# Optimization experiments

Measured on AMD Instinct MI355X. Metric: run time of the kernel, lower is better.

The kernel has to match this reference:

```python
import jax, jax.numpy as jnp
import numpy as np

B, T, D, H, C = 2048, 512, 1, 50, 2  # batch, seq_len, input_size, hidden_size, num_classes


def setup_inputs() -> dict:
    key = jax.random.key(0)
    ks = jax.random.split(key, 11)
    k = 1.0 / np.sqrt(H)  # torch default init bound
    u = lambda kk, shape: jax.random.uniform(kk, shape, jnp.float32, -k, k)
    return {
        "x": jax.random.normal(ks[0], (B, T, D), jnp.float32),
        "W_ih0": u(ks[1], (4 * H, D)),
        "W_hh0": u(ks[2], (4 * H, H)),
        "b_ih0": u(ks[3], (4 * H,)),
        "b_hh0": u(ks[4], (4 * H,)),
        "W_ih1": u(ks[5], (4 * H, H)),
        "W_hh1": u(ks[6], (4 * H, H)),
        "b_ih1": u(ks[7], (4 * H,)),
        "b_hh1": u(ks[8], (4 * H,)),
        "W_fc": u(ks[9], (C, H)),
        "b_fc": u(ks[10], (C,)),
    }


def _lstm_layer(x, Wih, Whh, bih, bhh):
    # x: [B, T, Din] -> hidden sequence [B, T, H]. PyTorch gate order: i, f, g, o.
    Bn = x.shape[0]
    Hn = Whh.shape[1]
    # precompute input contribution for all timesteps (one big GEMM)
    xg = jnp.einsum('btd,gd->btg', x, Wih) + bih + bhh  # [B, T, 4H]

    def step(carry, xg_t):
        h, c = carry
        g = xg_t + h @ Whh.T  # [B, 4H]
        i, f, gg, o = jnp.split(g, 4, axis=-1)
        i = jax.nn.sigmoid(i)
        f = jax.nn.sigmoid(f)
        gg = jnp.tanh(gg)
        o = jax.nn.sigmoid(o)
        c = f * c + i * gg
        h = o * jnp.tanh(c)
        return (h, c), h

    h0 = jnp.zeros((Bn, Hn), x.dtype)
    c0 = jnp.zeros((Bn, Hn), x.dtype)
    (_, _), hs = jax.lax.scan(step, (h0, c0), jnp.swapaxes(xg, 0, 1))  # hs: [T, B, H]
    return jnp.swapaxes(hs, 0, 1)


def reference(x, W_ih0, W_hh0, b_ih0, b_hh0, W_ih1, W_hh1, b_ih1, b_hh1, W_fc, b_fc):
    h1 = _lstm_layer(x, W_ih0, W_hh0, b_ih0, b_hh0)
    h2 = _lstm_layer(h1, W_ih1, W_hh1, b_ih1, b_hh1)
    # out[:, -1, :] @ W_fc.T + b_fc  (last-timestep hidden -> classifier)
    return h2[:, -1, :] @ W_fc.T + b_fc
```

## Files before the change

### kernel.cpp

```cpp
#include <hip/hip_runtime.h>

#define T_SEQ 512
#define HID   50
#define NB    8
#define BLK   832

typedef float v4f  __attribute__((ext_vector_type(4)));
typedef _Float16 f16;
typedef f16  f16x8 __attribute__((ext_vector_type(8)));


__device__ __forceinline__ f16x8 ldA0(const float* __restrict__ Whh0,
                                      const float* __restrict__ Wih0,
                                      const float* __restrict__ bih0,
                                      const float* __restrict__ bhh0,
                                      int m, int kb) {
    const int u = m >> 2, g = m & 3;
    f16x8 v;
    #pragma unroll
    for (int j = 0; j < 8; ++j) {
        const int k = kb + j;
        float f = 0.f;
        if (u < HID) {
            const int rho = g * HID + u;
            if (k < HID)      f = Whh0[rho * HID + k];
            else if (k == 62) f = Wih0[rho];
            else if (k == 63) f = bih0[rho] + bhh0[rho];
        }
        v[j] = (f16)f;
    }
    return v;
}

__device__ __forceinline__ f16x8 ldA1a(const float* __restrict__ Wih1,
                                       const float* __restrict__ bih1,
                                       const float* __restrict__ bhh1,
                                       int m, int kb) {
    const int u = m >> 2, g = m & 3;
    f16x8 v;
    #pragma unroll
    for (int j = 0; j < 8; ++j) {
        const int k = kb + j;
        float f = 0.f;
        if (u < HID) {
            const int rho = g * HID + u;
            if (k < HID)      f = Wih1[rho * HID + k];
            else if (k == 63) f = bih1[rho] + bhh1[rho];
        }
        v[j] = (f16)f;
    }
    return v;
}

__device__ __forceinline__ f16x8 ldA1b(const float* __restrict__ Whh1,
                                       int m, int kb) {
    const int u = m >> 2, g = m & 3;
    f16x8 v;
    #pragma unroll
    for (int j = 0; j < 8; ++j) {
        const int k = kb + j;
        float f = 0.f;
        if (u < HID && k < HID) f = Whh1[(g * HID + u) * HID + k];
        v[j] = (f16)f;
    }
    return v;
}

#define MFMA16(A, B, C) __builtin_amdgcn_mfma_f32_16x16x32_f16((A), (B), (C), 0, 0, 0)

__global__ __launch_bounds__(BLK, 1)
void lstm2_mfma(const float* __restrict__ x,
                const float* __restrict__ Wih0,
                const float* __restrict__ Whh0,
                const float* __restrict__ bih0,
                const float* __restrict__ bhh0,
                const float* __restrict__ Wih1,
                const float* __restrict__ Whh1,
                const float* __restrict__ bih1,
                const float* __restrict__ bhh1,
                const float* __restrict__ Wfc,
                const float* __restrict__ bfc,
                float* __restrict__ out)
{
    __shared__ __align__(16) f16 BPH [8 * 64 * 8];
    __shared__ f16   xs16[NB][T_SEQ];
    __shared__ float hfin[HID][NB];

    const int tid  = threadIdx.x;
    const int w    = tid >> 6;
    const int lane = tid & 63;
    const int n16  = lane & 15;
    const int quad = lane >> 4;
    const int bb0  = blockIdx.x * NB;

    const float* xg = x + (long)bb0 * T_SEQ;

    for (int i = tid; i < 8 * 64 * 8; i += BLK) BPH[i] = (f16)0.f;
    for (int i = tid; i < NB * T_SEQ; i += BLK) {
        const int n = i >> 9, tt = i & (T_SEQ - 1);
        xs16[n][tt] = (f16)xg[n * T_SEQ + tt];
    }

    const int m   = w * 16 + n16;
    const int kb0 = quad * 8, kb1 = 32 + quad * 8;
    const f16x8 a0 = ldA0(Whh0, Wih0, bih0, bhh0, m, kb0);
    const f16x8 a1 = ldA0(Whh0, Wih0, bih0, bhh0, m, kb1);
    const f16x8 v0 = ldA1a(Wih1, bih1, bhh1, m, kb0);
    const f16x8 v1 = ldA1a(Wih1, bih1, bhh1, m, kb1);
    const f16x8 v2 = ldA1b(Whh1, m, kb0);
    const f16x8 v3 = ldA1b(Whh1, m, kb1);

    __syncthreads();
    if (tid < NB) {
        BPH[(1 * 64 + 48 + tid) * 8 + 7] = (f16)1.f;
        BPH[(3 * 64 + 48 + tid) * 8 + 7] = (f16)1.f;
        BPH[(3 * 64 + 48 + tid) * 8 + 6] = xs16[tid][0];
    }
    __syncthreads();

    const int  u_    = w * 4 + quad;
    const bool isl0  = (n16 < 8);
    const bool valid = (u_ < HID);
    const int  wbase = ((u_ >> 5) * 64 + ((u_ & 31) >> 3) * 16 + (n16 & 7)) * 8 + (u_ & 7);
    float cs = 0.f;
    const f16x8* BPF = (const f16x8*)BPH;

    #pragma clang loop unroll(disable)
    for (int s = 0; s <= T_SEQ; ++s) {
        const int rb = (s + 1) & 1, wb = s & 1;

        const f16x8 B0 = BPF[(2 * rb + 0) * 64 + lane];
        const f16x8 B1 = BPF[(2 * rb + 1) * 64 + lane];
        const f16x8 B2 = BPF[(4 + 2 * wb + 0) * 64 + lane];
        const f16x8 B3 = BPF[(4 + 2 * wb + 1) * 64 + lane];

        v4f C0 = {0.f, 0.f, 0.f, 0.f};
        v4f C1 = {0.f, 0.f, 0.f, 0.f};
        C0 = MFMA16(a0, B0, C0);
        C0 = MFMA16(a1, B1, C0);
        C1 = MFMA16(v0, B0, C1);
        C1 = MFMA16(v1, B1, C1);
        C1 = MFMA16(v2, B2, C1);
        C1 = MFMA16(v3, B3, C1);

        const float sx = __shfl_xor(C1.x, 8);
        const float sy = __shfl_xor(C1.y, 8);
        const float sz = __shfl_xor(C1.z, 8);
        const float sw = __shfl_xor(C1.w, 8);
        v4f CC;
        CC.x = isl0 ? C0.x : sx;
        CC.y = isl0 ? C0.y : sy;
        CC.z = isl0 ? C0.z : sz;
        CC.w = isl0 ? C0.w : sw;

        const bool active = isl0 ? (s < T_SEQ) : (s >= 1);

        const float e1 = __expf(-CC.x);
        const float e2 = __expf(-CC.y);
        const float e3 = __expf(-2.f * CC.z);
        const float e4 = __expf(-CC.w);
        const float d1 = 1.f + e1, d2 = 1.f + e2, d3 = 1.f + e3, d4 = 1.f + e4;
        const float p2 = d1 * d2, p3 = p2 * d3, p4 = p3 * d4;
        const float i4 = __builtin_amdgcn_rcpf(p4);
        const float go = i4 * p3;
        const float i3 = i4 * d4;
        const float r3 = i3 * p2;
        const float i2 = i3 * d3;
        const float gf = i2 * d1;
        const float gi = i2 * d2;
        const float gg = fmaf(2.f, r3, -1.f);
        const float csn = fmaf(gf, cs, gi * gg);
        cs = active ? csn : cs;
        const float th = fmaf(2.f, __builtin_amdgcn_rcpf(1.f + __expf(-2.f * cs)), -1.f);
        const float hh = go * th;

        if (valid && active) {
            const int tb = isl0 ? (2 * wb) : (4 + 2 * rb);
            BPH[tb * 512 + wbase] = (f16)hh;
            if (!isl0 && s == T_SEQ) hfin[u_][n16 & 7] = hh;
        }

        if (w == 0 && lane < NB && s + 1 < T_SEQ)
            BPH[((2 * wb + 1) * 64 + 48 + lane) * 8 + 6] = xs16[lane][s + 1];

        __syncthreads();
    }

    if (tid < NB * 2) {
        const int nn = tid >> 1, c = tid & 1;
        float acc = bfc[c];
        #pragma unroll
        for (int u = 0; u < HID; ++u)
            acc = fmaf(Wfc[c * HID + u], hfin[u][nn], acc);
        out[(bb0 + nn) * 2 + c] = acc;
    }
}

extern "C" void kernel_launch(void* const* d_in, const int* in_sizes, int n_in,
                              void* d_out, int out_size, void* d_ws, size_t ws_size,
                              hipStream_t stream) {
    const float* x    = (const float*)d_in[0];
    const float* Wih0 = (const float*)d_in[1];
    const float* Whh0 = (const float*)d_in[2];
    const float* bih0 = (const float*)d_in[3];
    const float* bhh0 = (const float*)d_in[4];
    const float* Wih1 = (const float*)d_in[5];
    const float* Whh1 = (const float*)d_in[6];
    const float* bih1 = (const float*)d_in[7];
    const float* bhh1 = (const float*)d_in[8];
    const float* Wfc  = (const float*)d_in[9];
    const float* bfc  = (const float*)d_in[10];
    float* out = (float*)d_out;

    const int B = in_sizes[0] / T_SEQ;
    const int grid = B / NB;

    hipLaunchKernelGGL(lstm2_mfma, dim3(grid), dim3(BLK), 0, stream,
                       x, Wih0, Whh0, bih0, bhh0, Wih1, Whh1, bih1, bhh1,
                       Wfc, bfc, out);
}
```

Baseline: 378.7 us.

## Halve LDS B-operand buffers using DPP row-rotate and replace shuffles with DPP

Packs the two K-halves of each recurrent B operand into one LDS buffer, so each step loads one 16-byte vector per layer and builds the second half with a DPP row rotate by 8. The cross-lane exchange of layer-1 accumulators also moves from ds_bpermute-based shuffles to DPP row rotates. The aim is to cut LDS reads and shuffle latency on the serial recurrence critical path. In exchange it adds four DPP moves per operand and depends on the new layout matching the MFMA K-half mapping.

```diff
diff --git a/kernel.cpp b/kernel.cpp
--- a/kernel.cpp
+++ b/kernel.cpp
@@ -8,7 +8,22 @@
 typedef float v4f  __attribute__((ext_vector_type(4)));
 typedef _Float16 f16;
 typedef f16  f16x8 __attribute__((ext_vector_type(8)));
-
+typedef int  v4i  __attribute__((ext_vector_type(4)));
+
+
+__device__ __forceinline__ float ror8f(float v) {
+    return __builtin_bit_cast(float,
+        __builtin_amdgcn_update_dpp(0, __builtin_bit_cast(int, v),
+                                    0x128, 0xf, 0xf, false));
+}
+__device__ __forceinline__ f16x8 ror8x(f16x8 v) {
+    v4i a = __builtin_bit_cast(v4i, v); v4i r;
+    r.x = __builtin_amdgcn_update_dpp(0, a.x, 0x128, 0xf, 0xf, false);
+    r.y = __builtin_amdgcn_update_dpp(0, a.y, 0x128, 0xf, 0xf, false);
+    r.z = __builtin_amdgcn_update_dpp(0, a.z, 0x128, 0xf, 0xf, false);
+    r.w = __builtin_amdgcn_update_dpp(0, a.w, 0x128, 0xf, 0xf, false);
+    return __builtin_bit_cast(f16x8, r);
+}
 
 __device__ __forceinline__ f16x8 ldA0(const float* __restrict__ Whh0,
                                       const float* __restrict__ Wih0,
@@ -82,7 +97,7 @@
                 const float* __restrict__ bfc,
                 float* __restrict__ out)
 {
-    __shared__ __align__(16) f16 BPH [8 * 64 * 8];
+    __shared__ __align__(16) f16 BPH [4 * 64 * 8];
     __shared__ f16   xs16[NB][T_SEQ];
     __shared__ float hfin[HID][NB];
 
@@ -95,7 +110,7 @@
 
     const float* xg = x + (long)bb0 * T_SEQ;
 
-    for (int i = tid; i < 8 * 64 * 8; i += BLK) BPH[i] = (f16)0.f;
+    for (int i = tid; i < 4 * 64 * 8; i += BLK) BPH[i] = (f16)0.f;
     for (int i = tid; i < NB * T_SEQ; i += BLK) {
         const int n = i >> 9, tt = i & (T_SEQ - 1);
         xs16[n][tt] = (f16)xg[n * T_SEQ + tt];
@@ -112,16 +127,16 @@
 
     __syncthreads();
     if (tid < NB) {
-        BPH[(1 * 64 + 48 + tid) * 8 + 7] = (f16)1.f;
-        BPH[(3 * 64 + 48 + tid) * 8 + 7] = (f16)1.f;
-        BPH[(3 * 64 + 48 + tid) * 8 + 6] = xs16[tid][0];
+        BPH[(0 * 64 + 56 + tid) * 8 + 7] = (f16)1.f;
+        BPH[(1 * 64 + 56 + tid) * 8 + 7] = (f16)1.f;
+        BPH[(1 * 64 + 56 + tid) * 8 + 6] = xs16[tid][0];
     }
     __syncthreads();
 
     const int  u_    = w * 4 + quad;
     const bool isl0  = (n16 < 8);
     const bool valid = (u_ < HID);
-    const int  wbase = ((u_ >> 5) * 64 + ((u_ & 31) >> 3) * 16 + (n16 & 7)) * 8 + (u_ & 7);
+    const int  woff  = (((u_ & 31) >> 3) * 16 + (n16 & 7) + ((u_ >> 5) * 8)) * 8 + (u_ & 7);
     float cs = 0.f;
     const f16x8* BPF = (const f16x8*)BPH;
 
@@ -129,10 +144,12 @@
     for (int s = 0; s <= T_SEQ; ++s) {
         const int rb = (s + 1) & 1, wb = s & 1;
 
-        const f16x8 B0 = BPF[(2 * rb + 0) * 64 + lane];
-        const f16x8 B1 = BPF[(2 * rb + 1) * 64 + lane];
-        const f16x8 B2 = BPF[(4 + 2 * wb + 0) * 64 + lane];
-        const f16x8 B3 = BPF[(4 + 2 * wb + 1) * 64 + lane];
+        const f16x8 rA = BPF[rb * 64 + lane];
+        const f16x8 rB = BPF[(2 + wb) * 64 + lane];
+        const f16x8 B0 = rA;
+        const f16x8 B1 = ror8x(rA);
+        const f16x8 B2 = rB;
+        const f16x8 B3 = ror8x(rB);
 
         v4f C0 = {0.f, 0.f, 0.f, 0.f};
         v4f C1 = {0.f, 0.f, 0.f, 0.f};
@@ -143,10 +160,10 @@
         C1 = MFMA16(v2, B2, C1);
         C1 = MFMA16(v3, B3, C1);
 
-        const float sx = __shfl_xor(C1.x, 8);
-        const float sy = __shfl_xor(C1.y, 8);
-        const float sz = __shfl_xor(C1.z, 8);
-        const float sw = __shfl_xor(C1.w, 8);
+        const float sx = ror8f(C1.x);
+        const float sy = ror8f(C1.y);
+        const float sz = ror8f(C1.z);
+        const float sw = ror8f(C1.w);
         v4f CC;
         CC.x = isl0 ? C0.x : sx;
         CC.y = isl0 ? C0.y : sy;
@@ -175,13 +192,13 @@
         const float hh = go * th;
 
         if (valid && active) {
-            const int tb = isl0 ? (2 * wb) : (4 + 2 * rb);
-            BPH[tb * 512 + wbase] = (f16)hh;
+            const int buf = isl0 ? wb : (2 + rb);
+            BPH[buf * 512 + woff] = (f16)hh;
             if (!isl0 && s == T_SEQ) hfin[u_][n16 & 7] = hh;
         }
 
         if (w == 0 && lane < NB && s + 1 < T_SEQ)
-            BPH[((2 * wb + 1) * 64 + 48 + lane) * 8 + 6] = xs16[lane][s + 1];
+            BPH[(wb * 64 + 56 + lane) * 8 + 6] = xs16[lane][s + 1];
 
         __syncthreads();
     }
```

After: 438.0 us. +15.7%, slower.

## Duplicate hidden state across both batch column halves to drop cross-lane shuffles

Applied to the files above, without the earlier changes.

The B operand in shared memory now holds each batch's hidden state and x value in both column halves (columns 0-7 and 8-15), so every lane's MFMA output already holds the gates for its own batch. The four xor-8 shuffles are removed, and the layer-1 accumulation is split into two independent MFMA chains that are added at the end, which shortens the dependency chain. In exchange every h write and x write goes to shared memory twice, and the layer-1 sum costs an extra add.

```diff
diff --git a/kernel.cpp b/kernel.cpp
--- a/kernel.cpp
+++ b/kernel.cpp
@@ -113,17 +113,21 @@
     __syncthreads();
     if (tid < NB) {
         BPH[(1 * 64 + 48 + tid) * 8 + 7] = (f16)1.f;
+        BPH[(1 * 64 + 56 + tid) * 8 + 7] = (f16)1.f;
         BPH[(3 * 64 + 48 + tid) * 8 + 7] = (f16)1.f;
+        BPH[(3 * 64 + 56 + tid) * 8 + 7] = (f16)1.f;
         BPH[(3 * 64 + 48 + tid) * 8 + 6] = xs16[tid][0];
+        BPH[(3 * 64 + 56 + tid) * 8 + 6] = xs16[tid][0];
     }
     __syncthreads();
 
     const int  u_    = w * 4 + quad;
     const bool isl0  = (n16 < 8);
     const bool valid = (u_ < HID);
-    const int  wbase = ((u_ >> 5) * 64 + ((u_ & 31) >> 3) * 16 + (n16 & 7)) * 8 + (u_ & 7);
+    const int  wbase = (((u_ & 31) >> 3) * 16 + (n16 & 7)) * 8 + (u_ & 7) + (u_ >> 5) * 512;
     float cs = 0.f;
     const f16x8* BPF = (const f16x8*)BPH;
+    const v4f CZ = {0.f, 0.f, 0.f, 0.f};
 
     #pragma clang loop unroll(disable)
     for (int s = 0; s <= T_SEQ; ++s) {
@@ -134,24 +138,18 @@
         const f16x8 B2 = BPF[(4 + 2 * wb + 0) * 64 + lane];
         const f16x8 B3 = BPF[(4 + 2 * wb + 1) * 64 + lane];
 
-        v4f C0 = {0.f, 0.f, 0.f, 0.f};
-        v4f C1 = {0.f, 0.f, 0.f, 0.f};
-        C0 = MFMA16(a0, B0, C0);
+        v4f C0 = MFMA16(a0, B0, CZ);
         C0 = MFMA16(a1, B1, C0);
-        C1 = MFMA16(v0, B0, C1);
-        C1 = MFMA16(v1, B1, C1);
-        C1 = MFMA16(v2, B2, C1);
-        C1 = MFMA16(v3, B3, C1);
-
-        const float sx = __shfl_xor(C1.x, 8);
-        const float sy = __shfl_xor(C1.y, 8);
-        const float sz = __shfl_xor(C1.z, 8);
-        const float sw = __shfl_xor(C1.w, 8);
+        v4f C1h = MFMA16(v0, B0, CZ);
+        C1h = MFMA16(v1, B1, C1h);
+        v4f C1r = MFMA16(v2, B2, CZ);
+        C1r = MFMA16(v3, B3, C1r);
+
         v4f CC;
-        CC.x = isl0 ? C0.x : sx;
-        CC.y = isl0 ? C0.y : sy;
-        CC.z = isl0 ? C0.z : sz;
-        CC.w = isl0 ? C0.w : sw;
+        CC.x = isl0 ? C0.x : (C1h.x + C1r.x);
+        CC.y = isl0 ? C0.y : (C1h.y + C1r.y);
+        CC.z = isl0 ? C0.z : (C1h.z + C1r.z);
+        CC.w = isl0 ? C0.w : (C1h.w + C1r.w);
 
         const bool active = isl0 ? (s < T_SEQ) : (s >= 1);
 
@@ -176,12 +174,17 @@
 
         if (valid && active) {
             const int tb = isl0 ? (2 * wb) : (4 + 2 * rb);
-            BPH[tb * 512 + wbase] = (f16)hh;
+            f16* p = &BPH[tb * 512 + wbase];
+            p[0]  = (f16)hh;
+            p[64] = (f16)hh;
             if (!isl0 && s == T_SEQ) hfin[u_][n16 & 7] = hh;
         }
 
-        if (w == 0 && lane < NB && s + 1 < T_SEQ)
-            BPH[((2 * wb + 1) * 64 + 48 + lane) * 8 + 6] = xs16[lane][s + 1];
+        if (w == 0 && lane < NB && s + 1 < T_SEQ) {
+            const f16 xv = xs16[lane][s + 1];
+            BPH[((2 * wb + 1) * 64 + 48 + lane) * 8 + 6] = xv;
+            BPH[((2 * wb + 1) * 64 + 56 + lane) * 8 + 6] = xv;
+        }
 
         __syncthreads();
     }
```

After: 369.8 us. 1.02x faster.
